# Performance work log

Measured on AMD Instinct MI355X. Metric: run time of the kernel, lower is better.

Reference implementation:

```python
import jax, jax.numpy as jnp
import numpy as np

E, D, H, O, K = 8, 1024, 4096, 1024, 2
N = 4096


def setup_inputs() -> dict:
    key = jax.random.key(0)
    ks = jax.random.split(key, 8)
    s_in = 1.0 / np.sqrt(D)
    s_h = 1.0 / np.sqrt(H)
    return {
        "x": jax.random.normal(ks[0], (N, D), dtype=jnp.float32),
        "W1": jax.random.uniform(ks[1], (E, D, H), jnp.float32, -s_in, s_in),
        "b1": jax.random.uniform(ks[2], (E, H), jnp.float32, -s_in, s_in),
        "W2": jax.random.uniform(ks[3], (E, H, O), jnp.float32, -s_h, s_h),
        "b2": jax.random.uniform(ks[4], (E, O), jnp.float32, -s_h, s_h),
        "Wg": jax.random.uniform(ks[5], (D, E), jnp.float32, -s_in, s_in),
        "bg": jax.random.uniform(ks[6], (E,), jnp.float32, -s_in, s_in),
    }


def reference(x, W1, b1, W2, b2, Wg, bg):
    # gate: [N, E] -> top-k logits and expert ids
    gate_logits = x @ Wg + bg
    topv, topi = jax.lax.top_k(gate_logits, K)          # [N, K]
    weights = jax.nn.softmax(topv, axis=-1)             # softmax over the k selected logits

    # dense all-expert MLP, then gather the selected experts per token
    h = jax.nn.relu(jnp.einsum("nd,edh->enh", x, W1) + b1[:, None, :])  # [E, N, H]
    y = jnp.einsum("enh,eho->eno", h, W2) + b2[:, None, :]              # [E, N, O]

    sel = y[topi, jnp.arange(N)[:, None]]               # [N, K, O]
    return jnp.sum(weights[..., None] * sel, axis=1)    # [N, O]
```

## Files before the change

### kernel.cpp

```cpp
#include <hip/hip_runtime.h>
#include <hip/hip_bf16.h>
#include <cstdint>

typedef __bf16 bf16;
typedef bf16 bf16x8 __attribute__((ext_vector_type(8)));
typedef bf16 bf16x4 __attribute__((ext_vector_type(4)));
typedef float f32x4 __attribute__((ext_vector_type(4)));

#define N_TOK 4096
#define DIM   1024
#define HID   4096
#define OUTD  1024
#define NEXP  8
#define KSPLIT 4

__device__ __forceinline__ void async_copy16(const void* g, void* l) {
  __builtin_amdgcn_global_load_lds(
      (const __attribute__((address_space(1))) void*)g,
      (__attribute__((address_space(3))) void*)l, 16, 0, 0);
}

__global__ __launch_bounds__(256) void gate_kernel(
    const float* __restrict__ x, const float* __restrict__ Wg,
    const float* __restrict__ bg, int* __restrict__ topE, float* __restrict__ topW)
{
  int wave = threadIdx.x >> 6, lane = threadIdx.x & 63;
  int t = blockIdx.x * 4 + wave;
  float acc[8];
#pragma unroll
  for (int e = 0; e < 8; ++e) acc[e] = 0.f;
  const float* xrow = x + (size_t)t * DIM;
#pragma unroll
  for (int i = 0; i < DIM / 64; ++i) {
    int d = i * 64 + lane;
    float xv = xrow[d];
    float4 w0 = *(const float4*)(Wg + d * 8);
    float4 w1 = *(const float4*)(Wg + d * 8 + 4);
    acc[0] += xv * w0.x; acc[1] += xv * w0.y; acc[2] += xv * w0.z; acc[3] += xv * w0.w;
    acc[4] += xv * w1.x; acc[5] += xv * w1.y; acc[6] += xv * w1.z; acc[7] += xv * w1.w;
  }
#pragma unroll
  for (int off = 32; off > 0; off >>= 1) {
#pragma unroll
    for (int e = 0; e < 8; ++e) acc[e] += __shfl_xor(acc[e], off, 64);
  }
  if (lane == 0) {
    float l[8];
#pragma unroll
    for (int e = 0; e < 8; ++e) l[e] = acc[e] + bg[e];
    int e1 = 0;
#pragma unroll
    for (int e = 1; e < 8; ++e) if (l[e] > l[e1]) e1 = e;
    int e2 = (e1 == 0) ? 1 : 0;
#pragma unroll
    for (int e = 0; e < 8; ++e) if (e != e1 && l[e] > l[e2]) e2 = e;
    float w1 = 1.f / (1.f + __expf(l[e2] - l[e1]));
    topE[t * 2] = e1; topE[t * 2 + 1] = e2;
    topW[t * 2] = w1; topW[t * 2 + 1] = 1.f - w1;
  }
}

__global__ __launch_bounds__(256) void build_lists(
    const int* __restrict__ topE, const float* __restrict__ topW,
    int* __restrict__ cnt, int* __restrict__ tok_list, float* __restrict__ w_list)
{
  __shared__ int lcnt[8], lbase[8];
  int tid = threadIdx.x;
  if (tid < 8) lcnt[tid] = 0;
  __syncthreads();
  int t = blockIdx.x * 256 + tid;
  int e1 = topE[2 * t], e2 = topE[2 * t + 1];
  float w1 = topW[2 * t], w2 = topW[2 * t + 1];
  int p1 = atomicAdd(&lcnt[e1], 1);
  int p2 = atomicAdd(&lcnt[e2], 1);
  __syncthreads();
  if (tid < 8) lbase[tid] = atomicAdd(&cnt[tid], lcnt[tid]);
  __syncthreads();
  int i1 = e1 * N_TOK + lbase[e1] + p1;
  int i2 = e2 * N_TOK + lbase[e2] + p2;
  tok_list[i1] = t; w_list[i1] = w1;
  tok_list[i2] = t; w_list[i2] = w2;
}

__global__ void scan_kernel(const int* __restrict__ cnt, int* __restrict__ base)
{
  if (threadIdx.x == 0) {
    int s = 0;
    for (int e = 0; e < 8; ++e) { base[e] = s; s += cnt[e]; }
    base[8] = s;
  }
}

__global__ __launch_bounds__(256) void gather_cvt(
    const float* __restrict__ x, const int* __restrict__ tok_list,
    const int* __restrict__ base, bf16* __restrict__ xg)
{
  int wave = threadIdx.x >> 6, lane = threadIdx.x & 63;
  int s = blockIdx.x * 4 + wave;
  int e = 0;
#pragma unroll
  for (int i = 1; i < 8; ++i) e += (s >= base[i]);
  int tok = tok_list[e * N_TOK + (s - base[e])];
  const float4* src = (const float4*)(x + (size_t)tok * DIM);
  bf16x4* dst = (bf16x4*)(xg + (size_t)s * DIM);
#pragma unroll
  for (int i = 0; i < DIM / 256; ++i) {
    float4 v = src[i * 64 + lane];
    bf16x4 o;
    o.x = (bf16)v.x; o.y = (bf16)v.y; o.z = (bf16)v.z; o.w = (bf16)v.w;
    dst[i * 64 + lane] = o;
  }
}

__global__ __launch_bounds__(256) void transpose_cvt(
    const float* __restrict__ src, bf16* __restrict__ dst, int R, int C)
{
  __shared__ bf16 tile[64][65];
  int e = blockIdx.z;
  const float* s = src + (size_t)e * R * C;
  bf16* d = dst + (size_t)e * R * C;
  int c0 = blockIdx.x * 64, r0 = blockIdx.y * 64;
  int tid = threadIdx.x;
  int rr = tid >> 4;
  int cc = (tid & 15) * 4;
#pragma unroll
  for (int i = 0; i < 4; ++i) {
    int r = i * 16 + rr;
    float4 v = *(const float4*)(s + (size_t)(r0 + r) * C + c0 + cc);
    tile[cc + 0][r] = (bf16)v.x;
    tile[cc + 1][r] = (bf16)v.y;
    tile[cc + 2][r] = (bf16)v.z;
    tile[cc + 3][r] = (bf16)v.w;
  }
  __syncthreads();
#pragma unroll
  for (int i = 0; i < 4; ++i) {
    int ct = i * 16 + rr;
    bf16x4 o;
    o.x = tile[ct][cc + 0];
    o.y = tile[ct][cc + 1];
    o.z = tile[ct][cc + 2];
    o.w = tile[ct][cc + 3];
    *(bf16x4*)(d + (size_t)(c0 + ct) * R + r0 + cc) = o;
  }
}

__global__ __launch_bounds__(256) void gemm1_kernel(
    const bf16* __restrict__ xg, const bf16* __restrict__ W1t,
    const float* __restrict__ b1, bf16* __restrict__ hbuf,
    const int* __restrict__ cnt, const int* __restrict__ base)
{
  int e = blockIdx.z;
  int M = cnt[e];
  int mt = blockIdx.y;
  if (mt * 128 >= M) return;
  int nt = blockIdx.x;
  int b0 = base[e];

  __shared__ bf16 As[128 * 32];
  __shared__ bf16 Bs[128 * 32];

  int tid = threadIdx.x;
  int wave = tid >> 6, lane = tid & 63;

  int rA0 = wave * 32 + (lane >> 2);
  int rA1 = rA0 + 16;
  int kofs = (lane & 3) * 8;
  int lm0 = min(mt * 128 + rA0, M - 1);
  int lm1 = min(mt * 128 + rA1, M - 1);
  const bf16* gA0 = xg + (size_t)(b0 + lm0) * DIM + kofs;
  const bf16* gA1 = xg + (size_t)(b0 + lm1) * DIM + kofs;
  const bf16* gB0 = W1t + ((size_t)e * HID + nt * 128 + rA0) * DIM + kofs;
  const bf16* gB1 = W1t + ((size_t)e * HID + nt * 128 + rA1) * DIM + kofs;
  bf16* lA0 = As + (wave * 2 + 0) * 512;
  bf16* lA1 = As + (wave * 2 + 1) * 512;
  bf16* lB0 = Bs + (wave * 2 + 0) * 512;
  bf16* lB1 = Bs + (wave * 2 + 1) * 512;

  int wm = wave & 1, wn = wave >> 1;
  int quad = lane >> 4, lr = lane & 15;
  f32x4 acc[4][4] = {};

  for (int kt = 0; kt < DIM / 32; ++kt) {
    int ko = kt * 32;
    async_copy16(gA0 + ko, lA0);
    async_copy16(gA1 + ko, lA1);
    async_copy16(gB0 + ko, lB0);
    async_copy16(gB1 + ko, lB1);
    __syncthreads();
    bf16x8 af[4], bfr[4];
#pragma unroll
    for (int i = 0; i < 4; ++i)
      af[i] = *(const bf16x8*)(As + (wm * 64 + i * 16 + lr) * 32 + quad * 8);
#pragma unroll
    for (int j = 0; j < 4; ++j)
      bfr[j] = *(const bf16x8*)(Bs + (wn * 64 + j * 16 + lr) * 32 + quad * 8);
#pragma unroll
    for (int i = 0; i < 4; ++i)
#pragma unroll
      for (int j = 0; j < 4; ++j)
        acc[i][j] = __builtin_amdgcn_mfma_f32_16x16x32_bf16(af[i], bfr[j], acc[i][j], 0, 0, 0);
    __syncthreads();
  }

#pragma unroll
  for (int j = 0; j < 4; ++j) {
    int col = nt * 128 + wn * 64 + j * 16 + lr;
    float bias = b1[e * HID + col];
#pragma unroll
    for (int i = 0; i < 4; ++i) {
#pragma unroll
      for (int r = 0; r < 4; ++r) {
        int lm = mt * 128 + wm * 64 + i * 16 + quad * 4 + r;
        if (lm < M) {
          float v = acc[i][j][r] + bias;
          hbuf[(size_t)(b0 + lm) * HID + col] = (bf16)fmaxf(v, 0.f);
        }
      }
    }
  }
}

__global__ __launch_bounds__(256) void gemm2_kernel(
    const bf16* __restrict__ hbuf, const bf16* __restrict__ W2t,
    const float* __restrict__ b2, float* __restrict__ out,
    const int* __restrict__ cnt, const int* __restrict__ base,
    const int* __restrict__ tok_list, const float* __restrict__ w_list)
{
  int ez = blockIdx.z;
  int e = ez / KSPLIT;
  int ks = ez % KSPLIT;
  int M = cnt[e];
  int mt = blockIdx.y;
  if (mt * 128 >= M) return;
  int nt = blockIdx.x;
  int b0 = base[e];
  const int KC = HID / KSPLIT;
  int k0 = ks * KC;

  __shared__ bf16 As[128 * 32];
  __shared__ bf16 Bs[128 * 32];

  int tid = threadIdx.x;
  int wave = tid >> 6, lane = tid & 63;

  int rA0 = wave * 32 + (lane >> 2);
  int rA1 = rA0 + 16;
  int kofs = (lane & 3) * 8;
  int lm0 = min(mt * 128 + rA0, M - 1);
  int lm1 = min(mt * 128 + rA1, M - 1);
  const bf16* gA0 = hbuf + (size_t)(b0 + lm0) * HID + k0 + kofs;
  const bf16* gA1 = hbuf + (size_t)(b0 + lm1) * HID + k0 + kofs;
  const bf16* gB0 = W2t + ((size_t)e * OUTD + nt * 128 + rA0) * HID + k0 + kofs;
  const bf16* gB1 = W2t + ((size_t)e * OUTD + nt * 128 + rA1) * HID + k0 + kofs;
  bf16* lA0 = As + (wave * 2 + 0) * 512;
  bf16* lA1 = As + (wave * 2 + 1) * 512;
  bf16* lB0 = Bs + (wave * 2 + 0) * 512;
  bf16* lB1 = Bs + (wave * 2 + 1) * 512;

  int wm = wave & 1, wn = wave >> 1;
  int quad = lane >> 4, lr = lane & 15;
  f32x4 acc[4][4] = {};

  for (int kt = 0; kt < KC / 32; ++kt) {
    int ko = kt * 32;
    async_copy16(gA0 + ko, lA0);
    async_copy16(gA1 + ko, lA1);
    async_copy16(gB0 + ko, lB0);
    async_copy16(gB1 + ko, lB1);
    __syncthreads();
    bf16x8 af[4], bfr[4];
#pragma unroll
    for (int i = 0; i < 4; ++i)
      af[i] = *(const bf16x8*)(As + (wm * 64 + i * 16 + lr) * 32 + quad * 8);
#pragma unroll
    for (int j = 0; j < 4; ++j)
      bfr[j] = *(const bf16x8*)(Bs + (wn * 64 + j * 16 + lr) * 32 + quad * 8);
#pragma unroll
    for (int i = 0; i < 4; ++i)
#pragma unroll
      for (int j = 0; j < 4; ++j)
        acc[i][j] = __builtin_amdgcn_mfma_f32_16x16x32_bf16(af[i], bfr[j], acc[i][j], 0, 0, 0);
    __syncthreads();
  }

#pragma unroll
  for (int i = 0; i < 4; ++i) {
#pragma unroll
    for (int r = 0; r < 4; ++r) {
      int lm = mt * 128 + wm * 64 + i * 16 + quad * 4 + r;
      if (lm < M) {
        int tok = tok_list[e * N_TOK + lm];
        float w = w_list[e * N_TOK + lm];
#pragma unroll
        for (int j = 0; j < 4; ++j) {
          int col = nt * 128 + wn * 64 + j * 16 + lr;
          float v = acc[i][j][r];
          if (ks == 0) v += b2[e * OUTD + col];
          atomicAdd(out + (size_t)tok * OUTD + col, w * v);
        }
      }
    }
  }
}

extern "C" void kernel_launch(void* const* d_in, const int* in_sizes, int n_in,
                              void* d_out, int out_size, void* d_ws, size_t ws_size,
                              hipStream_t stream)
{
  (void)in_sizes; (void)n_in; (void)ws_size;
  const float* x  = (const float*)d_in[0];
  const float* W1 = (const float*)d_in[1];
  const float* b1 = (const float*)d_in[2];
  const float* W2 = (const float*)d_in[3];
  const float* b2 = (const float*)d_in[4];
  const float* Wg = (const float*)d_in[5];
  const float* bg = (const float*)d_in[6];
  float* out = (float*)d_out;

  char* ws = (char*)d_ws;
  int*   tok_list = (int*)(ws + 0);
  float* w_list   = (float*)(ws + 131072);
  int*   topE     = (int*)(ws + 262144);
  float* topW     = (float*)(ws + 294912);
  int*   cnt      = (int*)(ws + 327680);
  int*   base     = (int*)(ws + 327744);
  bf16*  xg   = (bf16*)(ws + 393216);
  bf16*  W1t  = (bf16*)(ws + 17170432);
  bf16*  hbuf = (bf16*)(ws + 84279296);
  bf16*  W2t  = (bf16*)(ws + 393216);

  hipMemsetAsync(d_out, 0, (size_t)out_size * sizeof(float), stream);
  hipMemsetAsync(cnt, 0, 64, stream);

  gate_kernel<<<dim3(N_TOK / 4), 256, 0, stream>>>(x, Wg, bg, topE, topW);
  build_lists<<<dim3(N_TOK / 256), 256, 0, stream>>>(topE, topW, cnt, tok_list, w_list);
  scan_kernel<<<dim3(1), 64, 0, stream>>>(cnt, base);
  gather_cvt<<<dim3(2 * N_TOK / 4), 256, 0, stream>>>(x, tok_list, base, xg);
  transpose_cvt<<<dim3(HID / 64, DIM / 64, NEXP), 256, 0, stream>>>(W1, W1t, DIM, HID);
  gemm1_kernel<<<dim3(HID / 128, N_TOK / 128, NEXP), 256, 0, stream>>>(xg, W1t, b1, hbuf, cnt, base);
  transpose_cvt<<<dim3(OUTD / 64, HID / 64, NEXP), 256, 0, stream>>>(W2, W2t, HID, OUTD);
  gemm2_kernel<<<dim3(OUTD / 128, N_TOK / 128, NEXP * KSPLIT), 256, 0, stream>>>(hbuf, W2t, b2, out, cnt, base, tok_list, w_list);
}
```

Before: 680.3 us.

## Replace split-K atomic scatter in gemm2 with per-slot buffers plus combine kernel

Drops the 4-way split-K in the second GEMM, whose epilogue scattered weighted results into the output with float atomics. Each routed slot's output row is now written once to a scratch buffer, and a new combine kernel takes the weighted sum of each token's two expert rows using an inverse index recorded in build_lists. This removes the output memset and the atomic traffic. The cost is fewer gemm2 blocks, since the grid shrinks by the split factor, which may leave CUs idle, plus an extra pass that writes and reads about 32 MB of fp32 scratch.

```diff
diff --git a/kernel.cpp b/kernel.cpp
--- a/kernel.cpp
+++ b/kernel.cpp
@@ -12,7 +12,6 @@
 #define HID   4096
 #define OUTD  1024
 #define NEXP  8
-#define KSPLIT 4
 
 __device__ __forceinline__ void async_copy16(const void* g, void* l) {
   __builtin_amdgcn_global_load_lds(
@@ -62,7 +61,8 @@
 
 __global__ __launch_bounds__(256) void build_lists(
     const int* __restrict__ topE, const float* __restrict__ topW,
-    int* __restrict__ cnt, int* __restrict__ tok_list, float* __restrict__ w_list)
+    int* __restrict__ cnt, int* __restrict__ tok_list, float* __restrict__ w_list,
+    int* __restrict__ inv)
 {
   __shared__ int lcnt[8], lbase[8];
   int tid = threadIdx.x;
@@ -80,6 +80,8 @@
   int i2 = e2 * N_TOK + lbase[e2] + p2;
   tok_list[i1] = t; w_list[i1] = w1;
   tok_list[i2] = t; w_list[i2] = w2;
+  inv[2 * t] = i1;
+  inv[2 * t + 1] = i2;
 }
 
 __global__ void scan_kernel(const int* __restrict__ cnt, int* __restrict__ base)
@@ -223,20 +225,15 @@
 
 __global__ __launch_bounds__(256) void gemm2_kernel(
     const bf16* __restrict__ hbuf, const bf16* __restrict__ W2t,
-    const float* __restrict__ b2, float* __restrict__ out,
-    const int* __restrict__ cnt, const int* __restrict__ base,
-    const int* __restrict__ tok_list, const float* __restrict__ w_list)
-{
-  int ez = blockIdx.z;
-  int e = ez / KSPLIT;
-  int ks = ez % KSPLIT;
+    const float* __restrict__ b2, float* __restrict__ ybufA, float* __restrict__ ybufB,
+    const int* __restrict__ cnt, const int* __restrict__ base)
+{
+  int e = blockIdx.z;
   int M = cnt[e];
   int mt = blockIdx.y;
   if (mt * 128 >= M) return;
   int nt = blockIdx.x;
   int b0 = base[e];
-  const int KC = HID / KSPLIT;
-  int k0 = ks * KC;
 
   __shared__ bf16 As[128 * 32];
   __shared__ bf16 Bs[128 * 32];
@@ -249,10 +246,10 @@
   int kofs = (lane & 3) * 8;
   int lm0 = min(mt * 128 + rA0, M - 1);
   int lm1 = min(mt * 128 + rA1, M - 1);
-  const bf16* gA0 = hbuf + (size_t)(b0 + lm0) * HID + k0 + kofs;
-  const bf16* gA1 = hbuf + (size_t)(b0 + lm1) * HID + k0 + kofs;
-  const bf16* gB0 = W2t + ((size_t)e * OUTD + nt * 128 + rA0) * HID + k0 + kofs;
-  const bf16* gB1 = W2t + ((size_t)e * OUTD + nt * 128 + rA1) * HID + k0 + kofs;
+  const bf16* gA0 = hbuf + (size_t)(b0 + lm0) * HID + kofs;
+  const bf16* gA1 = hbuf + (size_t)(b0 + lm1) * HID + kofs;
+  const bf16* gB0 = W2t + ((size_t)e * OUTD + nt * 128 + rA0) * HID + kofs;
+  const bf16* gB1 = W2t + ((size_t)e * OUTD + nt * 128 + rA1) * HID + kofs;
   bf16* lA0 = As + (wave * 2 + 0) * 512;
   bf16* lA1 = As + (wave * 2 + 1) * 512;
   bf16* lB0 = Bs + (wave * 2 + 0) * 512;
@@ -262,7 +259,7 @@
   int quad = lane >> 4, lr = lane & 15;
   f32x4 acc[4][4] = {};
 
-  for (int kt = 0; kt < KC / 32; ++kt) {
+  for (int kt = 0; kt < HID / 32; ++kt) {
     int ko = kt * 32;
     async_copy16(gA0 + ko, lA0);
     async_copy16(gA1 + ko, lA1);
@@ -285,30 +282,59 @@
   }
 
 #pragma unroll
-  for (int i = 0; i < 4; ++i) {
-#pragma unroll
-    for (int r = 0; r < 4; ++r) {
-      int lm = mt * 128 + wm * 64 + i * 16 + quad * 4 + r;
-      if (lm < M) {
-        int tok = tok_list[e * N_TOK + lm];
-        float w = w_list[e * N_TOK + lm];
-#pragma unroll
-        for (int j = 0; j < 4; ++j) {
-          int col = nt * 128 + wn * 64 + j * 16 + lr;
-          float v = acc[i][j][r];
-          if (ks == 0) v += b2[e * OUTD + col];
-          atomicAdd(out + (size_t)tok * OUTD + col, w * v);
+  for (int j = 0; j < 4; ++j) {
+    int col = nt * 128 + wn * 64 + j * 16 + lr;
+    float bias = b2[e * OUTD + col];
+#pragma unroll
+    for (int i = 0; i < 4; ++i) {
+#pragma unroll
+      for (int r = 0; r < 4; ++r) {
+        int lm = mt * 128 + wm * 64 + i * 16 + quad * 4 + r;
+        if (lm < M) {
+          int slot = b0 + lm;
+          float* yr = (slot < 4096) ? (ybufA + (size_t)slot * OUTD)
+                                    : (ybufB + (size_t)(slot - 4096) * OUTD);
+          yr[col] = acc[i][j][r] + bias;
         }
       }
     }
   }
 }
 
+__global__ __launch_bounds__(256) void combine_kernel(
+    const float* __restrict__ ybufA, const float* __restrict__ ybufB,
+    const int* __restrict__ inv, const float* __restrict__ topW,
+    const int* __restrict__ base, float* __restrict__ out)
+{
+  int wave = threadIdx.x >> 6, lane = threadIdx.x & 63;
+  int t = blockIdx.x * 4 + wave;
+  int i0 = inv[2 * t], i1 = inv[2 * t + 1];
+  float w0 = topW[2 * t], w1 = topW[2 * t + 1];
+  int s0 = base[i0 >> 12] + (i0 & (N_TOK - 1));
+  int s1 = base[i1 >> 12] + (i1 & (N_TOK - 1));
+  const float4* r0 = (const float4*)((s0 < 4096) ? (ybufA + (size_t)s0 * OUTD)
+                                                 : (ybufB + (size_t)(s0 - 4096) * OUTD));
+  const float4* r1 = (const float4*)((s1 < 4096) ? (ybufA + (size_t)s1 * OUTD)
+                                                 : (ybufB + (size_t)(s1 - 4096) * OUTD));
+  float4* o = (float4*)(out + (size_t)t * OUTD);
+#pragma unroll
+  for (int i = 0; i < OUTD / 256; ++i) {
+    float4 a = r0[i * 64 + lane];
+    float4 b = r1[i * 64 + lane];
+    float4 c;
+    c.x = w0 * a.x + w1 * b.x;
+    c.y = w0 * a.y + w1 * b.y;
+    c.z = w0 * a.z + w1 * b.z;
+    c.w = w0 * a.w + w1 * b.w;
+    o[i * 64 + lane] = c;
+  }
+}
+
 extern "C" void kernel_launch(void* const* d_in, const int* in_sizes, int n_in,
                               void* d_out, int out_size, void* d_ws, size_t ws_size,
                               hipStream_t stream)
 {
-  (void)in_sizes; (void)n_in; (void)ws_size;
+  (void)in_sizes; (void)n_in; (void)ws_size; (void)out_size;
   const float* x  = (const float*)d_in[0];
   const float* W1 = (const float*)d_in[1];
   const float* b1 = (const float*)d_in[2];
@@ -325,20 +351,23 @@
   float* topW     = (float*)(ws + 294912);
   int*   cnt      = (int*)(ws + 327680);
   int*   base     = (int*)(ws + 327744);
-  bf16*  xg   = (bf16*)(ws + 393216);
-  bf16*  W1t  = (bf16*)(ws + 17170432);
-  bf16*  hbuf = (bf16*)(ws + 84279296);
-  bf16*  W2t  = (bf16*)(ws + 393216);
-
-  hipMemsetAsync(d_out, 0, (size_t)out_size * sizeof(float), stream);
+  int*   inv      = (int*)(ws + 327808);
+  bf16*  xg    = (bf16*)(ws + 393216);
+  bf16*  W1t   = (bf16*)(ws + 17170432);
+  bf16*  hbuf  = (bf16*)(ws + 84279296);
+  bf16*  W2t   = (bf16*)(ws + 393216);
+  float* ybufA = (float*)(ws + 67502080);
+  float* ybufB = (float*)(ws + 151388160);
+
   hipMemsetAsync(cnt, 0, 64, stream);
 
   gate_kernel<<<dim3(N_TOK / 4), 256, 0, stream>>>(x, Wg, bg, topE, topW);
-  build_lists<<<dim3(N_TOK / 256), 256, 0, stream>>>(topE, topW, cnt, tok_list, w_list);
+  build_lists<<<dim3(N_TOK / 256), 256, 0, stream>>>(topE, topW, cnt, tok_list, w_list, inv);
   scan_kernel<<<dim3(1), 64, 0, stream>>>(cnt, base);
   gather_cvt<<<dim3(2 * N_TOK / 4), 256, 0, stream>>>(x, tok_list, base, xg);
   transpose_cvt<<<dim3(HID / 64, DIM / 64, NEXP), 256, 0, stream>>>(W1, W1t, DIM, HID);
   gemm1_kernel<<<dim3(HID / 128, N_TOK / 128, NEXP), 256, 0, stream>>>(xg, W1t, b1, hbuf, cnt, base);
   transpose_cvt<<<dim3(OUTD / 64, HID / 64, NEXP), 256, 0, stream>>>(W2, W2t, HID, OUTD);
-  gemm2_kernel<<<dim3(OUTD / 128, N_TOK / 128, NEXP * KSPLIT), 256, 0, stream>>>(hbuf, W2t, b2, out, cnt, base, tok_list, w_list);
-}
+  gemm2_kernel<<<dim3(OUTD / 128, N_TOK / 128, NEXP), 256, 0, stream>>>(hbuf, W2t, b2, ybufA, ybufB, cnt, base);
+  combine_kernel<<<dim3(N_TOK / 4), 256, 0, stream>>>(ybufA, ybufB, inv, topW, base, out);
+}
```

Result: faster. 588.4 us (-13.5%).
